# Optimization experiments

Measured on AMD Instinct MI355X. Metric: run time of the kernel, lower is better.

## Reference

```python
import jax, jax.numpy as jnp
import numpy as np

H = 64          # nheads
NH = 8          # lru_dim // nheads (per-head state dim, must be even)
LRU_DIM = 512
HIDDEN = 512
BATCH = 8
T = 4096
MAX_PHASE = 6.28
R_MIN, R_MAX = 0.9, 0.999


def setup_inputs() -> dict:
    key = jax.random.key(0)
    ks = jax.random.split(key, 8)
    input_sequence = jax.random.normal(ks[0], (BATCH, 1, HIDDEN, 1, T), dtype=jnp.float32)
    # theta_init: log(uniform(0, max_phase)), shape (lru_dim//2, 1)
    theta_log = jnp.log(jax.random.uniform(ks[1], (LRU_DIM // 2, 1), maxval=MAX_PHASE))
    # ortho_mat_init(lru_dim, N)
    P = jax.random.normal(ks[2], (LRU_DIM, NH)) / jnp.sqrt(NH + LRU_DIM)
    # mat_init(lru_dim, hidden_dim)
    B = jax.random.normal(ks[3], (LRU_DIM, HIDDEN)) / jnp.sqrt(HIDDEN + LRU_DIM)
    # mat_init(hidden_dim, lru_dim)
    C = jax.random.normal(ks[4], (HIDDEN, LRU_DIM)) / jnp.sqrt(HIDDEN + LRU_DIM)
    D = jax.random.normal(ks[5], (HIDDEN,))
    # nu_log_init: log(-log r) interpolated by uniform
    u1 = jax.random.uniform(ks[6], (H,))
    gamma_log = jnp.log(-jnp.log(R_MAX)) + u1 * (jnp.log(-jnp.log(R_MIN)) - jnp.log(-jnp.log(R_MAX)))
    return dict(input_sequence=input_sequence, theta_log=theta_log, P=P, B=B, C=C, D=D,
                gamma_log=gamma_log)


def _mix_sequence(gamma, thetas, Us):
    """Single head. gamma: scalar, thetas: (N/2,), Us: (T, B, N) -> (T, B, N)."""
    def binf(a, b):
        g_i, th_i, acc_i = a
        g_j, th_j, acc_j = b
        # rotate-half (RoPE-style) of accumulated state
        rot = jnp.stack([-acc_i[..., 1::2], acc_i[..., 0::2]], axis=-1).reshape(acc_i.shape)
        theta = jnp.repeat(th_j[..., None], 2, axis=-1).reshape(th_j.shape[:-1] + (th_j.shape[-1] * 2,))
        sin = jnp.sin(theta)[..., None, :]  # (..., 1, N)
        cos = jnp.cos(theta)[..., None, :]
        acc = g_j[..., None, None] * (cos * acc_i + sin * rot)
        return (g_i * g_j, th_i + th_j, acc + acc_j)

    Tlen = Us.shape[0]
    gammas = jnp.repeat(gamma[None], Tlen, axis=0)          # (T,)
    Rs = jnp.repeat(thetas[None, :], Tlen, axis=0)          # (T, N/2)
    _, _, res = jax.lax.associative_scan(binf, (gammas, Rs, Us))
    return res


def reference(input_sequence, theta_log, P, B, C, D, gamma_log):
    x = input_sequence[:, 0, :, 0].transpose(0, 2, 1)       # (B, T, hidden)
    bsz, Tlen, _ = x.shape
    thetas = jnp.exp(theta_log.reshape(H, NH // 2))          # (H, N/2)
    Pm = P.reshape(H, NH, NH)
    Bm = B.reshape(H, NH, HIDDEN)
    gamma = jnp.exp(-jnp.exp(gamma_log))                     # (H,)
    # trace(B B^T) per head == sum of squares
    trace_per_head = jnp.sum(Bm * Bm, axis=(1, 2))
    norm = jnp.sqrt((1.0 - gamma ** 2) / trace_per_head)
    B_norm = norm[:, None, None] * Bm                        # (H, N, hidden)
    # orthogonalize P via matrix exponential of skew-symmetric part
    Pm = jax.vmap(jax.scipy.linalg.expm)(Pm - Pm.transpose(0, 2, 1))  # (H, N, N)
    Us = jnp.einsum('HnD,BTD->HTBn', B_norm, x)              # project inputs per head
    Us = jnp.einsum('HnN,HTBn->HTBN', Pm.transpose(0, 2, 1), Us)
    y = jax.vmap(_mix_sequence)(gamma, thetas, Us)           # (H, T, B, N)
    y = jnp.einsum('HNn,HTBN->HTBn', Pm, y)
    y = y.transpose(2, 1, 0, 3).reshape(bsz, Tlen, -1)       # (B, T, lru_dim)
    y = jnp.einsum('Dn,BTn->BTD', C, y) + D * x
    return y[0]                                              # (T, hidden)
```

## Files before the change

### kernel.cpp

```cpp
#include <hip/hip_runtime.h>
#include <math.h>

#define NHEADS   64
#define TLEN     4096
#define CHUNK    16
#define NCHUNK   256

typedef unsigned short u16;
typedef unsigned int   u32;
typedef __attribute__((ext_vector_type(8))) short bf16x8;
typedef __attribute__((ext_vector_type(4))) float f32x4;

__device__ __forceinline__ u16 f2bf(float x) {
    u32 u = __float_as_uint(x);
    u32 r = (u + 0x7FFFu + ((u >> 16) & 1u)) >> 16;
    return (u16)r;
}
__device__ __forceinline__ float bf2f(u16 h) { return __uint_as_float(((u32)h) << 16); }


__global__ void k_setup(const float* __restrict__ P,
                        const float* __restrict__ Bmat,
                        const float* __restrict__ theta_log,
                        const float* __restrict__ gamma_log,
                        float* __restrict__ ws) {
    __shared__ double As[8][8];
    __shared__ double Rs[8][8];
    __shared__ double red[64];
    __shared__ int sh_s;
    const int h = blockIdx.x;
    const int tid = threadIdx.x;
    const int i = tid >> 3, j = tid & 7;

    As[i][j] = (double)P[(h*8 + i)*8 + j] - (double)P[(h*8 + j)*8 + i];

    const float* Bh = Bmat + h*8*512;
    double ss = 0.0;
    for (int q = 0; q < 64; ++q) { float v = Bh[q*64 + tid]; ss += (double)v * (double)v; }
    red[tid] = ss;
    __syncthreads();

    if (tid == 0) {
        double nrm = 0.0;
        for (int r = 0; r < 8; ++r) {
            double rs = 0.0;
            for (int c = 0; c < 8; ++c) rs += fabs(As[r][c]);
            nrm = fmax(nrm, rs);
        }
        int s = 0;
        while (nrm > 0.25 && s < 40) { nrm *= 0.5; ++s; }
        sh_s = s;
        double tr = 0.0;
        for (int q = 0; q < 64; ++q) tr += red[q];
        double ed = exp((double)gamma_log[h]);
        double g  = exp(-ed);
        ws[4096 + h] = (float)g;
        ws[4416 + h] = (float)sqrt((1.0 - g*g) / tr);
    }
    if (tid < 4) ws[4160 + h*4 + tid] = expf(theta_log[h*4 + tid]);
    __syncthreads();

    const double sc = ldexp(1.0, -sh_s);
    As[i][j] *= sc;
    const int NT = 13;
    Rs[i][j] = (i == j ? 1.0 : 0.0) + As[i][j] / (double)NT;
    __syncthreads();
    for (int k = NT - 1; k >= 1; --k) {
        double t = 0.0;
        #pragma unroll
        for (int m = 0; m < 8; ++m) t += As[i][m] * Rs[m][j];
        __syncthreads();
        Rs[i][j] = (i == j ? 1.0 : 0.0) + t / (double)k;
        __syncthreads();
    }
    for (int q = 0; q < sh_s; ++q) {
        double t = 0.0;
        #pragma unroll
        for (int m = 0; m < 8; ++m) t += Rs[i][m] * Rs[m][j];
        __syncthreads();
        Rs[i][j] = t;
        __syncthreads();
    }
    ws[h*64 + i*8 + j] = (float)Rs[i][j];
}

__global__ void k_proj(const float* __restrict__ Bmat,
                       const float* __restrict__ C,
                       const float* __restrict__ ws_ro,
                       u16* __restrict__ W1pk,
                       u16* __restrict__ CEpk) {
    const int gid = blockIdx.x * 256 + threadIdx.x;
    if (gid < 512*512) {
        const int k = gid >> 9, d = gid & 511;
        const int h = k >> 3, N = k & 7;
        const float* Pm = ws_ro + h*64 + N*8;
        const float nrm = ws_ro[4416 + h];
        float acc = 0.f;
        #pragma unroll
        for (int n = 0; n < 8; ++n) acc += Pm[n] * Bmat[(h*8 + n)*512 + d];
        acc *= nrm;
        u16 hi = f2bf(acc), lo = f2bf(acc - bf2f(hi));
        W1pk[k*1024 + d] = hi;
        W1pk[k*1024 + 512 + d] = lo;
    } else {
        const int g2 = gid - 512*512;
        const int e = g2 >> 9, k = g2 & 511;
        const int h = k >> 3, N = k & 7;
        const float* Pm = ws_ro + h*64 + N*8;
        float acc = 0.f;
        #pragma unroll
        for (int n = 0; n < 8; ++n) acc += Pm[n] * C[e*512 + h*8 + n];
        u16 hi = f2bf(acc), lo = f2bf(acc - bf2f(hi));
        CEpk[e*1024 + k] = hi;
        CEpk[e*1024 + 512 + k] = lo;
    }
}

__global__ void k_xt(const float* __restrict__ X, u16* __restrict__ XT) {
    __shared__ float Xs[64][65];
    const int tid = threadIdx.x;
    const int t0 = blockIdx.x * 64, d0 = blockIdx.y * 64;
    {
        const int dr = tid >> 4, tc = (tid & 15) * 4;
        #pragma unroll
        for (int it = 0; it < 4; ++it) {
            const int dd = it*16 + dr;
            float4 v = *reinterpret_cast<const float4*>(X + (size_t)(d0 + dd)*4096 + t0 + tc);
            Xs[dd][tc] = v.x; Xs[dd][tc+1] = v.y; Xs[dd][tc+2] = v.z; Xs[dd][tc+3] = v.w;
        }
    }
    __syncthreads();
    const int tr = tid >> 2, ds = (tid & 3) * 16;
    u32 hb[8], lb[8];
    #pragma unroll
    for (int j = 0; j < 16; j += 2) {
        float a = Xs[ds + j][tr], b = Xs[ds + j + 1][tr];
        u16 ha = f2bf(a), la = f2bf(a - bf2f(ha));
        u16 hbb = f2bf(b), lbb = f2bf(b - bf2f(hbb));
        hb[j >> 1] = (u32)ha | ((u32)hbb << 16);
        lb[j >> 1] = (u32)la | ((u32)lbb << 16);
    }
    u16* orow = XT + (size_t)(t0 + tr)*1024 + d0 + ds;
    uint4 h0; h0.x = hb[0]; h0.y = hb[1]; h0.z = hb[2]; h0.w = hb[3];
    uint4 h1; h1.x = hb[4]; h1.y = hb[5]; h1.z = hb[6]; h1.w = hb[7];
    uint4 l0; l0.x = lb[0]; l0.y = lb[1]; l0.z = lb[2]; l0.w = lb[3];
    uint4 l1; l1.x = lb[4]; l1.y = lb[5]; l1.z = lb[6]; l1.w = lb[7];
    *reinterpret_cast<uint4*>(orow)       = h0;
    *reinterpret_cast<uint4*>(orow + 8)   = h1;
    *reinterpret_cast<uint4*>(orow + 512) = l0;
    *reinterpret_cast<uint4*>(orow + 520) = l1;
}

#define MFMA_BF16(A_, B_, C_) __builtin_amdgcn_mfma_f32_16x16x32_bf16(A_, B_, C_, 0, 0, 0)
template<int MODE>
__global__ __launch_bounds__(256) void k_gemm(const u16* __restrict__ Apk,
                                              const float* __restrict__ Af,
                                              const u16* __restrict__ Bpk,
                                              float* __restrict__ Cout,
                                              const u16* __restrict__ XT,
                                              const float* __restrict__ Dvec,
                                              const float* __restrict__ wsro,
                                              float* __restrict__ E,
                                              const float* __restrict__ S,
                                              const float* __restrict__ TAB) {
    __shared__ char smem[36864];
    u16* Ah = (u16*)smem;
    u16* Al = Ah + 4608;
    u16* Bh = Al + 4608;
    u16* Bl = Bh + 4608;
    float* Ut = (float*)smem;

    const int tid = threadIdx.x;
    const int bid = blockIdx.x;
    const int tile = (bid & 7) * 64 + (bid >> 3);
    const int mt = tile >> 3, nt = tile & 7;
    const int m0 = mt * 64, n0 = nt * 64;
    const int lane = tid & 63, wid = tid >> 6;
    const int wm = wid >> 1, wn = wid & 1;
    const int lr = lane & 15, lc = lane >> 4;
    const int sr = tid >> 2, ss = (tid & 3) * 16;

    f32x4 acc00 = {0.f,0.f,0.f,0.f}, acc01 = acc00, acc10 = acc00, acc11 = acc00;

    const int tA = m0 + sr;
    const int cA = tA >> 4, iA = tA & 15;
    const u16* Brow = Bpk + (size_t)(n0 + sr)*1024 + ss;
    const u16* Arow = (MODE == 0) ? (Apk + (size_t)tA*1024 + ss) : (const u16*)0;
    const float* Urow = (MODE == 1) ? (Af + (size_t)tA*512 + ss) : (const float*)0;

    for (int k0 = 0; k0 < 512; k0 += 64) {
        float4 vbh0 = *reinterpret_cast<const float4*>(Brow + k0);
        float4 vbh1 = *reinterpret_cast<const float4*>(Brow + k0 + 8);
        float4 vbl0 = *reinterpret_cast<const float4*>(Brow + 512 + k0);
        float4 vbl1 = *reinterpret_cast<const float4*>(Brow + 512 + k0 + 8);
        if constexpr (MODE == 0) {
            float4 vah0 = *reinterpret_cast<const float4*>(Arow + k0);
            float4 vah1 = *reinterpret_cast<const float4*>(Arow + k0 + 8);
            float4 val0 = *reinterpret_cast<const float4*>(Arow + 512 + k0);
            float4 val1 = *reinterpret_cast<const float4*>(Arow + 512 + k0 + 8);
            *reinterpret_cast<float4*>(&Ah[sr*72 + ss])     = vah0;
            *reinterpret_cast<float4*>(&Ah[sr*72 + ss + 8]) = vah1;
            *reinterpret_cast<float4*>(&Al[sr*72 + ss])     = val0;
            *reinterpret_cast<float4*>(&Al[sr*72 + ss + 8]) = val1;
        } else {
            const int p0 = (k0 + ss) >> 1;
            #pragma unroll
            for (int j = 0; j < 4; ++j) {
                float4 u = *reinterpret_cast<const float4*>(Urow + k0 + 4*j);
                float4 tb = *reinterpret_cast<const float4*>(TAB + ((size_t)iA*256 + p0 + 2*j)*2);
                float4 sv = *reinterpret_cast<const float4*>(S + (size_t)cA*512 + 2*p0 + 4*j);
                u.x += tb.x*sv.x - tb.y*sv.y;
                u.y += tb.y*sv.x + tb.x*sv.y;
                u.z += tb.z*sv.z - tb.w*sv.w;
                u.w += tb.w*sv.z + tb.z*sv.w;
                u16 hx = f2bf(u.x), hy = f2bf(u.y), hz = f2bf(u.z), hw = f2bf(u.w);
                u16 lx = f2bf(u.x - bf2f(hx)), ly = f2bf(u.y - bf2f(hy));
                u16 lz = f2bf(u.z - bf2f(hz)), lw = f2bf(u.w - bf2f(hw));
                uint2 wh; wh.x = (u32)hx | ((u32)hy << 16); wh.y = (u32)hz | ((u32)hw << 16);
                uint2 wl; wl.x = (u32)lx | ((u32)ly << 16); wl.y = (u32)lz | ((u32)lw << 16);
                *reinterpret_cast<uint2*>(&Ah[sr*72 + ss + 4*j]) = wh;
                *reinterpret_cast<uint2*>(&Al[sr*72 + ss + 4*j]) = wl;
            }
        }
        *reinterpret_cast<float4*>(&Bh[sr*72 + ss])     = vbh0;
        *reinterpret_cast<float4*>(&Bh[sr*72 + ss + 8]) = vbh1;
        *reinterpret_cast<float4*>(&Bl[sr*72 + ss])     = vbl0;
        *reinterpret_cast<float4*>(&Bl[sr*72 + ss + 8]) = vbl1;
        __syncthreads();
        #pragma unroll
        for (int kk = 0; kk < 2; ++kk) {
            const int ko = kk*32 + lc*8;
            const int ra0 = (wm*32 + lr)*72 + ko,  ra1 = ra0 + 16*72;
            const int rb0 = (wn*32 + lr)*72 + ko,  rb1 = rb0 + 16*72;
            bf16x8 fah0 = *reinterpret_cast<const bf16x8*>(&Ah[ra0]);
            bf16x8 fah1 = *reinterpret_cast<const bf16x8*>(&Ah[ra1]);
            bf16x8 fal0 = *reinterpret_cast<const bf16x8*>(&Al[ra0]);
            bf16x8 fal1 = *reinterpret_cast<const bf16x8*>(&Al[ra1]);
            bf16x8 fbh0 = *reinterpret_cast<const bf16x8*>(&Bh[rb0]);
            bf16x8 fbh1 = *reinterpret_cast<const bf16x8*>(&Bh[rb1]);
            bf16x8 fbl0 = *reinterpret_cast<const bf16x8*>(&Bl[rb0]);
            bf16x8 fbl1 = *reinterpret_cast<const bf16x8*>(&Bl[rb1]);
            acc00 = MFMA_BF16(fah0, fbl0, acc00);
            acc00 = MFMA_BF16(fal0, fbh0, acc00);
            acc00 = MFMA_BF16(fah0, fbh0, acc00);
            acc01 = MFMA_BF16(fah0, fbl1, acc01);
            acc01 = MFMA_BF16(fal0, fbh1, acc01);
            acc01 = MFMA_BF16(fah0, fbh1, acc01);
            acc10 = MFMA_BF16(fah1, fbl0, acc10);
            acc10 = MFMA_BF16(fal1, fbh0, acc10);
            acc10 = MFMA_BF16(fah1, fbh0, acc10);
            acc11 = MFMA_BF16(fah1, fbl1, acc11);
            acc11 = MFMA_BF16(fal1, fbh1, acc11);
            acc11 = MFMA_BF16(fah1, fbh1, acc11);
        }
        __syncthreads();
    }

    if constexpr (MODE == 0) {
        #pragma unroll
        for (int im = 0; im < 2; ++im) {
            #pragma unroll
            for (int in = 0; in < 2; ++in) {
                f32x4 v = (im == 0) ? (in == 0 ? acc00 : acc01)
                                    : (in == 0 ? acc10 : acc11);
                const int row0 = wm*32 + im*16 + lc*4;
                const int col  = wn*32 + in*16 + lr;
                #pragma unroll
                for (int rg = 0; rg < 4; ++rg)
                    Ut[(row0 + rg)*72 + col] = v[rg];
            }
        }
        __syncthreads();
        if (tid < 128) {
            const int cc = tid >> 5, pp = tid & 31;
            const int pg = nt*32 + pp;
            const float th = wsro[4160 + pg];
            const float g  = wsro[4096 + (pg >> 2)];
            const float cs = cosf(th), sn = sinf(th);
            float h0 = 0.f, h1 = 0.f;
            float* col = Ut + (cc*16)*72 + 2*pp;
            #pragma unroll
            for (int i = 0; i < CHUNK; ++i) {
                float a = col[i*72], b = col[i*72 + 1];
                float n0v = g*(cs*h0 - sn*h1) + a;
                float n1v = g*(sn*h0 + cs*h1) + b;
                col[i*72] = n0v; col[i*72 + 1] = n1v;
                h0 = n0v; h1 = n1v;
            }
            E[(size_t)(mt*4 + cc)*512 + 2*pg]     = h0;
            E[(size_t)(mt*4 + cc)*512 + 2*pg + 1] = h1;
        }
        __syncthreads();
        const int row = tid >> 2, cseg = (tid & 3) * 16;
        #pragma unroll
        for (int j = 0; j < 4; ++j) {
            float4 v = *reinterpret_cast<const float4*>(&Ut[row*72 + cseg + 4*j]);
            *reinterpret_cast<float4*>(Cout + (size_t)(m0 + row)*512 + n0 + cseg + 4*j) = v;
        }
    } else {
        #pragma unroll
        for (int im = 0; im < 2; ++im) {
            #pragma unroll
            for (int in = 0; in < 2; ++in) {
                f32x4 v = (im == 0) ? (in == 0 ? acc00 : acc01)
                                    : (in == 0 ? acc10 : acc11);
                const int row0 = m0 + wm*32 + im*16 + lc*4;
                const int col  = n0 + wn*32 + in*16 + lr;
                const float dv = Dvec[col];
                #pragma unroll
                for (int rg = 0; rg < 4; ++rg) {
                    const int t = row0 + rg;
                    float xv = bf2f(XT[(size_t)t*1024 + col]) + bf2f(XT[(size_t)t*1024 + 512 + col]);
                    Cout[(size_t)t*512 + col] = v[rg] + dv*xv;
                }
            }
        }
    }
}

__global__ void k_carry(const float* __restrict__ E, float* __restrict__ S,
                        float* __restrict__ TAB,
                        const float* __restrict__ theta_log,
                        const float* __restrict__ gamma_log) {
    const int p = threadIdx.x;
    const double th = exp((double)theta_log[p]);
    const double ed = exp((double)gamma_log[p >> 2]);
    const double g  = exp(-ed);
    const double cd = cos(th), sd = sin(th);
    double gc = g*cd, gs = g*sd;
    for (int i = 0; i < CHUNK; ++i) {
        if (i) {
            double t0 = g*(cd*gc - sd*gs);
            double t1 = g*(sd*gc + cd*gs);
            gc = t0; gs = t1;
        }
        TAB[(i*256 + p)*2 + 0] = (float)gc;
        TAB[(i*256 + p)*2 + 1] = (float)gs;
    }
    const float fLc = (float)gc, fLs = (float)gs;
    float s0 = 0.f, s1 = 0.f;
    S[2*p] = 0.f; S[2*p + 1] = 0.f;
    const float* Ep = E + 2*p;
    float* Sp = S + 2*p;
    float2 bA[16], bB[16];
    #pragma unroll
    for (int j = 0; j < 16; ++j) bA[j] = *reinterpret_cast<const float2*>(Ep + (size_t)j*512);
    for (int bb = 0; bb < 8; ++bb) {
        const int b0 = 2*bb, b1 = 2*bb + 1;
        #pragma unroll
        for (int j = 0; j < 16; ++j)
            bB[j] = *reinterpret_cast<const float2*>(Ep + (size_t)(b1*16 + j)*512);
        #pragma unroll
        for (int j = 0; j < 16; ++j) {
            const int c = b0*16 + j + 1;
            float n0 = fLc*s0 - fLs*s1 + bA[j].x;
            float n1 = fLs*s0 + fLc*s1 + bA[j].y;
            s0 = n0; s1 = n1;
            *reinterpret_cast<float2*>(Sp + (size_t)c*512) = make_float2(s0, s1);
        }
        if (b1 + 1 < 16) {
            #pragma unroll
            for (int j = 0; j < 16; ++j)
                bA[j] = *reinterpret_cast<const float2*>(Ep + (size_t)((b1 + 1)*16 + j)*512);
        }
        #pragma unroll
        for (int j = 0; j < 16; ++j) {
            const int c = b1*16 + j + 1;
            float n0 = fLc*s0 - fLs*s1 + bB[j].x;
            float n1 = fLs*s0 + fLc*s1 + bB[j].y;
            s0 = n0; s1 = n1;
            if (c < NCHUNK)
                *reinterpret_cast<float2*>(Sp + (size_t)c*512) = make_float2(s0, s1);
        }
    }
}

extern "C" void kernel_launch(void* const* d_in, const int* in_sizes, int n_in,
                              void* d_out, int out_size, void* d_ws, size_t ws_size,
                              hipStream_t stream) {
    const float* X  = (const float*)d_in[0];
    const float* th = (const float*)d_in[1];
    const float* P  = (const float*)d_in[2];
    const float* Bm = (const float*)d_in[3];
    const float* C  = (const float*)d_in[4];
    const float* Dv = (const float*)d_in[5];
    const float* gl = (const float*)d_in[6];
    char* wsb = (char*)d_ws;
    float* ws   = (float*)wsb;
    u16*   W1pk = (u16*)(wsb + 32768);
    u16*   CEpk = (u16*)(wsb + 1081344);
    u16*   XTpk = (u16*)(wsb + 2129920);
    float* U    = (float*)(wsb + 10518528);
    float* E    = (float*)(wsb + 18907136);
    float* S    = (float*)(wsb + 19431424);
    float* TAB  = (float*)(wsb + 19955712);
    float* out  = (float*)d_out;

    k_setup<<<NHEADS, 64, 0, stream>>>(P, Bm, th, gl, ws);
    k_proj<<<2048, 256, 0, stream>>>(Bm, C, ws, W1pk, CEpk);
    k_xt<<<dim3(64, 8), 256, 0, stream>>>(X, XTpk);
    k_gemm<0><<<512, 256, 0, stream>>>(XTpk, (const float*)0, W1pk, U, XTpk, Dv, ws, E, S, TAB);
    k_carry<<<1, 256, 0, stream>>>(E, S, TAB, th, gl);
    k_gemm<1><<<512, 256, 0, stream>>>((const u16*)0, U, CEpk, out, XTpk, Dv, ws, E, S, TAB);
}
```

Measured before the change: 161.0 us.

## Parallelize chunk carry scan, fuse setup with transpose, prefetch GEMM tiles

The single-block serial carry recurrence over 256 chunks becomes a 64-block kernel with one wavefront per state pair. It runs a wave-level Kogge-Stone scan using shuffles and computes decay powers in closed form. The setup and input-transpose kernels merge into one launch, and the GEMM main loop register-prefetches the next K tile while MFMA runs on the current one. These target the serial latency of the carry kernel, one launch overhead, and global-load stalls in the GEMM. The trade-offs are extra transcendental work and slightly different float rounding in the scan.

Result: faster. 149.1 us (-7.4%).

```diff
diff --git a/kernel.cpp b/kernel.cpp
--- a/kernel.cpp
+++ b/kernel.cpp
@@ -19,24 +19,62 @@
 __device__ __forceinline__ float bf2f(u16 h) { return __uint_as_float(((u32)h) << 16); }
 
 
-__global__ void k_setup(const float* __restrict__ P,
-                        const float* __restrict__ Bmat,
-                        const float* __restrict__ theta_log,
-                        const float* __restrict__ gamma_log,
-                        float* __restrict__ ws) {
+__global__ void k_pre(const float* __restrict__ X, u16* __restrict__ XT,
+                      const float* __restrict__ P,
+                      const float* __restrict__ Bmat,
+                      const float* __restrict__ theta_log,
+                      const float* __restrict__ gamma_log,
+                      float* __restrict__ ws) {
+    const int tid = threadIdx.x;
+    if (blockIdx.x < 512) {
+        __shared__ float Xs[64][65];
+        const int t0 = (blockIdx.x & 63) * 64, d0 = (blockIdx.x >> 6) * 64;
+        {
+            const int dr = tid >> 4, tc = (tid & 15) * 4;
+            #pragma unroll
+            for (int it = 0; it < 4; ++it) {
+                const int dd = it*16 + dr;
+                float4 v = *reinterpret_cast<const float4*>(X + (size_t)(d0 + dd)*4096 + t0 + tc);
+                Xs[dd][tc] = v.x; Xs[dd][tc+1] = v.y; Xs[dd][tc+2] = v.z; Xs[dd][tc+3] = v.w;
+            }
+        }
+        __syncthreads();
+        const int tr = tid >> 2, ds = (tid & 3) * 16;
+        u32 hb[8], lb[8];
+        #pragma unroll
+        for (int j = 0; j < 16; j += 2) {
+            float a = Xs[ds + j][tr], b = Xs[ds + j + 1][tr];
+            u16 ha = f2bf(a), la = f2bf(a - bf2f(ha));
+            u16 hbb = f2bf(b), lbb = f2bf(b - bf2f(hbb));
+            hb[j >> 1] = (u32)ha | ((u32)hbb << 16);
+            lb[j >> 1] = (u32)la | ((u32)lbb << 16);
+        }
+        u16* orow = XT + (size_t)(t0 + tr)*1024 + d0 + ds;
+        uint4 h0; h0.x = hb[0]; h0.y = hb[1]; h0.z = hb[2]; h0.w = hb[3];
+        uint4 h1; h1.x = hb[4]; h1.y = hb[5]; h1.z = hb[6]; h1.w = hb[7];
+        uint4 l0; l0.x = lb[0]; l0.y = lb[1]; l0.z = lb[2]; l0.w = lb[3];
+        uint4 l1; l1.x = lb[4]; l1.y = lb[5]; l1.z = lb[6]; l1.w = lb[7];
+        *reinterpret_cast<uint4*>(orow)       = h0;
+        *reinterpret_cast<uint4*>(orow + 8)   = h1;
+        *reinterpret_cast<uint4*>(orow + 512) = l0;
+        *reinterpret_cast<uint4*>(orow + 520) = l1;
+        return;
+    }
     __shared__ double As[8][8];
     __shared__ double Rs[8][8];
-    __shared__ double red[64];
+    __shared__ double red[256];
     __shared__ int sh_s;
-    const int h = blockIdx.x;
-    const int tid = threadIdx.x;
-    const int i = tid >> 3, j = tid & 7;
-
-    As[i][j] = (double)P[(h*8 + i)*8 + j] - (double)P[(h*8 + j)*8 + i];
+    const int h = blockIdx.x - 512;
+    const int i = (tid & 63) >> 3, j = tid & 7;
+    const bool act = tid < 64;
+
+    if (act)
+        As[i][j] = (double)P[(h*8 + i)*8 + j] - (double)P[(h*8 + j)*8 + i];
 
     const float* Bh = Bmat + h*8*512;
     double ss = 0.0;
-    for (int q = 0; q < 64; ++q) { float v = Bh[q*64 + tid]; ss += (double)v * (double)v; }
+    #pragma unroll
+    for (int q = 0; q < 16; ++q) { float v = Bh[q*256 + tid]; ss += (double)v * (double)v; }
     red[tid] = ss;
     __syncthreads();
 
@@ -51,7 +89,7 @@
         while (nrm > 0.25 && s < 40) { nrm *= 0.5; ++s; }
         sh_s = s;
         double tr = 0.0;
-        for (int q = 0; q < 64; ++q) tr += red[q];
+        for (int q = 0; q < 256; ++q) tr += red[q];
         double ed = exp((double)gamma_log[h]);
         double g  = exp(-ed);
         ws[4096 + h] = (float)g;
@@ -60,28 +98,35 @@
     if (tid < 4) ws[4160 + h*4 + tid] = expf(theta_log[h*4 + tid]);
     __syncthreads();
 
-    const double sc = ldexp(1.0, -sh_s);
-    As[i][j] *= sc;
     const int NT = 13;
-    Rs[i][j] = (i == j ? 1.0 : 0.0) + As[i][j] / (double)NT;
+    if (act) {
+        const double sc = ldexp(1.0, -sh_s);
+        As[i][j] *= sc;
+        Rs[i][j] = (i == j ? 1.0 : 0.0) + As[i][j] / (double)NT;
+    }
     __syncthreads();
     for (int k = NT - 1; k >= 1; --k) {
         double t = 0.0;
-        #pragma unroll
-        for (int m = 0; m < 8; ++m) t += As[i][m] * Rs[m][j];
-        __syncthreads();
-        Rs[i][j] = (i == j ? 1.0 : 0.0) + t / (double)k;
-        __syncthreads();
-    }
-    for (int q = 0; q < sh_s; ++q) {
+        if (act) {
+            #pragma unroll
+            for (int m = 0; m < 8; ++m) t += As[i][m] * Rs[m][j];
+        }
+        __syncthreads();
+        if (act) Rs[i][j] = (i == j ? 1.0 : 0.0) + t / (double)k;
+        __syncthreads();
+    }
+    const int nsq = sh_s;
+    for (int q = 0; q < nsq; ++q) {
         double t = 0.0;
-        #pragma unroll
-        for (int m = 0; m < 8; ++m) t += Rs[i][m] * Rs[m][j];
-        __syncthreads();
-        Rs[i][j] = t;
-        __syncthreads();
-    }
-    ws[h*64 + i*8 + j] = (float)Rs[i][j];
+        if (act) {
+            #pragma unroll
+            for (int m = 0; m < 8; ++m) t += Rs[i][m] * Rs[m][j];
+        }
+        __syncthreads();
+        if (act) Rs[i][j] = t;
+        __syncthreads();
+    }
+    if (act) ws[h*64 + i*8 + j] = (float)Rs[i][j];
 }
 
 __global__ void k_proj(const float* __restrict__ Bmat,
@@ -114,41 +159,6 @@
         CEpk[e*1024 + k] = hi;
         CEpk[e*1024 + 512 + k] = lo;
     }
-}
-
-__global__ void k_xt(const float* __restrict__ X, u16* __restrict__ XT) {
-    __shared__ float Xs[64][65];
-    const int tid = threadIdx.x;
-    const int t0 = blockIdx.x * 64, d0 = blockIdx.y * 64;
-    {
-        const int dr = tid >> 4, tc = (tid & 15) * 4;
-        #pragma unroll
-        for (int it = 0; it < 4; ++it) {
-            const int dd = it*16 + dr;
-            float4 v = *reinterpret_cast<const float4*>(X + (size_t)(d0 + dd)*4096 + t0 + tc);
-            Xs[dd][tc] = v.x; Xs[dd][tc+1] = v.y; Xs[dd][tc+2] = v.z; Xs[dd][tc+3] = v.w;
-        }
-    }
-    __syncthreads();
-    const int tr = tid >> 2, ds = (tid & 3) * 16;
-    u32 hb[8], lb[8];
-    #pragma unroll
-    for (int j = 0; j < 16; j += 2) {
-        float a = Xs[ds + j][tr], b = Xs[ds + j + 1][tr];
-        u16 ha = f2bf(a), la = f2bf(a - bf2f(ha));
-        u16 hbb = f2bf(b), lbb = f2bf(b - bf2f(hbb));
-        hb[j >> 1] = (u32)ha | ((u32)hbb << 16);
-        lb[j >> 1] = (u32)la | ((u32)lbb << 16);
-    }
-    u16* orow = XT + (size_t)(t0 + tr)*1024 + d0 + ds;
-    uint4 h0; h0.x = hb[0]; h0.y = hb[1]; h0.z = hb[2]; h0.w = hb[3];
-    uint4 h1; h1.x = hb[4]; h1.y = hb[5]; h1.z = hb[6]; h1.w = hb[7];
-    uint4 l0; l0.x = lb[0]; l0.y = lb[1]; l0.z = lb[2]; l0.w = lb[3];
-    uint4 l1; l1.x = lb[4]; l1.y = lb[5]; l1.z = lb[6]; l1.w = lb[7];
-    *reinterpret_cast<uint4*>(orow)       = h0;
-    *reinterpret_cast<uint4*>(orow + 8)   = h1;
-    *reinterpret_cast<uint4*>(orow + 512) = l0;
-    *reinterpret_cast<uint4*>(orow + 520) = l1;
 }
 
 #define MFMA_BF16(A_, B_, C_) __builtin_amdgcn_mfma_f32_16x16x32_bf16(A_, B_, C_, 0, 0, 0)
@@ -188,27 +198,42 @@
     const u16* Arow = (MODE == 0) ? (Apk + (size_t)tA*1024 + ss) : (const u16*)0;
     const float* Urow = (MODE == 1) ? (Af + (size_t)tA*512 + ss) : (const float*)0;
 
-    for (int k0 = 0; k0 < 512; k0 += 64) {
-        float4 vbh0 = *reinterpret_cast<const float4*>(Brow + k0);
-        float4 vbh1 = *reinterpret_cast<const float4*>(Brow + k0 + 8);
-        float4 vbl0 = *reinterpret_cast<const float4*>(Brow + 512 + k0);
-        float4 vbl1 = *reinterpret_cast<const float4*>(Brow + 512 + k0 + 8);
+    float4 rb0, rb1, rb2, rb3;
+    float4 ra0, ra1, ra2, ra3;
+    float4 ru[4], rtb[4], rsv[4];
+
+    {
+        const int k0 = 0;
+        rb0 = *reinterpret_cast<const float4*>(Brow + k0);
+        rb1 = *reinterpret_cast<const float4*>(Brow + k0 + 8);
+        rb2 = *reinterpret_cast<const float4*>(Brow + 512 + k0);
+        rb3 = *reinterpret_cast<const float4*>(Brow + 512 + k0 + 8);
         if constexpr (MODE == 0) {
-            float4 vah0 = *reinterpret_cast<const float4*>(Arow + k0);
-            float4 vah1 = *reinterpret_cast<const float4*>(Arow + k0 + 8);
-            float4 val0 = *reinterpret_cast<const float4*>(Arow + 512 + k0);
-            float4 val1 = *reinterpret_cast<const float4*>(Arow + 512 + k0 + 8);
-            *reinterpret_cast<float4*>(&Ah[sr*72 + ss])     = vah0;
-            *reinterpret_cast<float4*>(&Ah[sr*72 + ss + 8]) = vah1;
-            *reinterpret_cast<float4*>(&Al[sr*72 + ss])     = val0;
-            *reinterpret_cast<float4*>(&Al[sr*72 + ss + 8]) = val1;
+            ra0 = *reinterpret_cast<const float4*>(Arow + k0);
+            ra1 = *reinterpret_cast<const float4*>(Arow + k0 + 8);
+            ra2 = *reinterpret_cast<const float4*>(Arow + 512 + k0);
+            ra3 = *reinterpret_cast<const float4*>(Arow + 512 + k0 + 8);
         } else {
             const int p0 = (k0 + ss) >> 1;
             #pragma unroll
             for (int j = 0; j < 4; ++j) {
-                float4 u = *reinterpret_cast<const float4*>(Urow + k0 + 4*j);
-                float4 tb = *reinterpret_cast<const float4*>(TAB + ((size_t)iA*256 + p0 + 2*j)*2);
-                float4 sv = *reinterpret_cast<const float4*>(S + (size_t)cA*512 + 2*p0 + 4*j);
+                ru[j]  = *reinterpret_cast<const float4*>(Urow + k0 + 4*j);
+                rtb[j] = *reinterpret_cast<const float4*>(TAB + ((size_t)iA*256 + p0 + 2*j)*2);
+                rsv[j] = *reinterpret_cast<const float4*>(S + (size_t)cA*512 + 2*p0 + 4*j);
+            }
+        }
+    }
+
+    for (int s = 0; s < 8; ++s) {
+        if constexpr (MODE == 0) {
+            *reinterpret_cast<float4*>(&Ah[sr*72 + ss])     = ra0;
+            *reinterpret_cast<float4*>(&Ah[sr*72 + ss + 8]) = ra1;
+            *reinterpret_cast<float4*>(&Al[sr*72 + ss])     = ra2;
+            *reinterpret_cast<float4*>(&Al[sr*72 + ss + 8]) = ra3;
+        } else {
+            #pragma unroll
+            for (int j = 0; j < 4; ++j) {
+                float4 u = ru[j], tb = rtb[j], sv = rsv[j];
                 u.x += tb.x*sv.x - tb.y*sv.y;
                 u.y += tb.y*sv.x + tb.x*sv.y;
                 u.z += tb.z*sv.z - tb.w*sv.w;
@@ -222,24 +247,47 @@
                 *reinterpret_cast<uint2*>(&Al[sr*72 + ss + 4*j]) = wl;
             }
         }
-        *reinterpret_cast<float4*>(&Bh[sr*72 + ss])     = vbh0;
-        *reinterpret_cast<float4*>(&Bh[sr*72 + ss + 8]) = vbh1;
-        *reinterpret_cast<float4*>(&Bl[sr*72 + ss])     = vbl0;
-        *reinterpret_cast<float4*>(&Bl[sr*72 + ss + 8]) = vbl1;
-        __syncthreads();
+        *reinterpret_cast<float4*>(&Bh[sr*72 + ss])     = rb0;
+        *reinterpret_cast<float4*>(&Bh[sr*72 + ss + 8]) = rb1;
+        *reinterpret_cast<float4*>(&Bl[sr*72 + ss])     = rb2;
+        *reinterpret_cast<float4*>(&Bl[sr*72 + ss + 8]) = rb3;
+        __syncthreads();
+
+        if (s < 7) {
+            const int k0 = (s + 1) * 64;
+            rb0 = *reinterpret_cast<const float4*>(Brow + k0);
+            rb1 = *reinterpret_cast<const float4*>(Brow + k0 + 8);
+            rb2 = *reinterpret_cast<const float4*>(Brow + 512 + k0);
+            rb3 = *reinterpret_cast<const float4*>(Brow + 512 + k0 + 8);
+            if constexpr (MODE == 0) {
+                ra0 = *reinterpret_cast<const float4*>(Arow + k0);
+                ra1 = *reinterpret_cast<const float4*>(Arow + k0 + 8);
+                ra2 = *reinterpret_cast<const float4*>(Arow + 512 + k0);
+                ra3 = *reinterpret_cast<const float4*>(Arow + 512 + k0 + 8);
+            } else {
+                const int p0 = (k0 + ss) >> 1;
+                #pragma unroll
+                for (int j = 0; j < 4; ++j) {
+                    ru[j]  = *reinterpret_cast<const float4*>(Urow + k0 + 4*j);
+                    rtb[j] = *reinterpret_cast<const float4*>(TAB + ((size_t)iA*256 + p0 + 2*j)*2);
+                    rsv[j] = *reinterpret_cast<const float4*>(S + (size_t)cA*512 + 2*p0 + 4*j);
+                }
+            }
+        }
+
         #pragma unroll
         for (int kk = 0; kk < 2; ++kk) {
             const int ko = kk*32 + lc*8;
-            const int ra0 = (wm*32 + lr)*72 + ko,  ra1 = ra0 + 16*72;
-            const int rb0 = (wn*32 + lr)*72 + ko,  rb1 = rb0 + 16*72;
-            bf16x8 fah0 = *reinterpret_cast<const bf16x8*>(&Ah[ra0]);
-            bf16x8 fah1 = *reinterpret_cast<const bf16x8*>(&Ah[ra1]);
-            bf16x8 fal0 = *reinterpret_cast<const bf16x8*>(&Al[ra0]);
-            bf16x8 fal1 = *reinterpret_cast<const bf16x8*>(&Al[ra1]);
-            bf16x8 fbh0 = *reinterpret_cast<const bf16x8*>(&Bh[rb0]);
-            bf16x8 fbh1 = *reinterpret_cast<const bf16x8*>(&Bh[rb1]);
-            bf16x8 fbl0 = *reinterpret_cast<const bf16x8*>(&Bl[rb0]);
-            bf16x8 fbl1 = *reinterpret_cast<const bf16x8*>(&Bl[rb1]);
+            const int ra0i = (wm*32 + lr)*72 + ko,  ra1i = ra0i + 16*72;
+            const int rb0i = (wn*32 + lr)*72 + ko,  rb1i = rb0i + 16*72;
+            bf16x8 fah0 = *reinterpret_cast<const bf16x8*>(&Ah[ra0i]);
+            bf16x8 fah1 = *reinterpret_cast<const bf16x8*>(&Ah[ra1i]);
+            bf16x8 fal0 = *reinterpret_cast<const bf16x8*>(&Al[ra0i]);
+            bf16x8 fal1 = *reinterpret_cast<const bf16x8*>(&Al[ra1i]);
+            bf16x8 fbh0 = *reinterpret_cast<const bf16x8*>(&Bh[rb0i]);
+            bf16x8 fbh1 = *reinterpret_cast<const bf16x8*>(&Bh[rb1i]);
+            bf16x8 fbl0 = *reinterpret_cast<const bf16x8*>(&Bl[rb0i]);
+            bf16x8 fbl1 = *reinterpret_cast<const bf16x8*>(&Bl[rb1i]);
             acc00 = MFMA_BF16(fah0, fbl0, acc00);
             acc00 = MFMA_BF16(fal0, fbh0, acc00);
             acc00 = MFMA_BF16(fah0, fbh0, acc00);
@@ -322,57 +370,56 @@
                         float* __restrict__ TAB,
                         const float* __restrict__ theta_log,
                         const float* __restrict__ gamma_log) {
-    const int p = threadIdx.x;
+    const int w = threadIdx.x >> 6, l = threadIdx.x & 63;
+    const int p = blockIdx.x*4 + w;
     const double th = exp((double)theta_log[p]);
     const double ed = exp((double)gamma_log[p >> 2]);
-    const double g  = exp(-ed);
-    const double cd = cos(th), sd = sin(th);
-    double gc = g*cd, gs = g*sd;
-    for (int i = 0; i < CHUNK; ++i) {
-        if (i) {
-            double t0 = g*(cd*gc - sd*gs);
-            double t1 = g*(sd*gc + cd*gs);
-            gc = t0; gs = t1;
-        }
-        TAB[(i*256 + p)*2 + 0] = (float)gc;
-        TAB[(i*256 + p)*2 + 1] = (float)gs;
-    }
-    const float fLc = (float)gc, fLs = (float)gs;
-    float s0 = 0.f, s1 = 0.f;
-    S[2*p] = 0.f; S[2*p + 1] = 0.f;
+
+    if (l < CHUNK) {
+        double a = (double)(l + 1) * th;
+        double g = exp(-(double)(l + 1) * ed);
+        TAB[((size_t)l*256 + p)*2 + 0] = (float)(g * cos(a));
+        TAB[((size_t)l*256 + p)*2 + 1] = (float)(g * sin(a));
+    }
+
+    const double a16 = 16.0*th, g16 = exp(-16.0*ed);
+    const float Lc = (float)(g16*cos(a16)), Ls = (float)(g16*sin(a16));
+
     const float* Ep = E + 2*p;
+    float2 e0 = *reinterpret_cast<const float2*>(Ep + (size_t)(4*l + 0)*512);
+    float2 e1 = *reinterpret_cast<const float2*>(Ep + (size_t)(4*l + 1)*512);
+    float2 e2 = *reinterpret_cast<const float2*>(Ep + (size_t)(4*l + 2)*512);
+    float2 e3 = *reinterpret_cast<const float2*>(Ep + (size_t)(4*l + 3)*512);
+
+    float2 v = e0;
+    v = make_float2(Lc*v.x - Ls*v.y + e1.x, Ls*v.x + Lc*v.y + e1.y);
+    v = make_float2(Lc*v.x - Ls*v.y + e2.x, Ls*v.x + Lc*v.y + e2.y);
+    v = make_float2(Lc*v.x - Ls*v.y + e3.x, Ls*v.x + Lc*v.y + e3.y);
+
+    #pragma unroll
+    for (int d = 0; d < 6; ++d) {
+        const int sh = 1 << d;
+        const double aa = 64.0 * (double)sh * th;
+        const double gg = exp(-64.0 * (double)sh * ed);
+        const float Mc = (float)(gg*cos(aa)), Ms = (float)(gg*sin(aa));
+        float px = __shfl_up(v.x, sh, 64);
+        float py = __shfl_up(v.y, sh, 64);
+        if (l >= sh) {
+            v.x += Mc*px - Ms*py;
+            v.y += Ms*px + Mc*py;
+        }
+    }
+
+    float sx = __shfl_up(v.x, 1, 64), sy = __shfl_up(v.y, 1, 64);
+    float2 s = (l == 0) ? make_float2(0.f, 0.f) : make_float2(sx, sy);
     float* Sp = S + 2*p;
-    float2 bA[16], bB[16];
-    #pragma unroll
-    for (int j = 0; j < 16; ++j) bA[j] = *reinterpret_cast<const float2*>(Ep + (size_t)j*512);
-    for (int bb = 0; bb < 8; ++bb) {
-        const int b0 = 2*bb, b1 = 2*bb + 1;
-        #pragma unroll
-        for (int j = 0; j < 16; ++j)
-            bB[j] = *reinterpret_cast<const float2*>(Ep + (size_t)(b1*16 + j)*512);
-        #pragma unroll
-        for (int j = 0; j < 16; ++j) {
-            const int c = b0*16 + j + 1;
-            float n0 = fLc*s0 - fLs*s1 + bA[j].x;
-            float n1 = fLs*s0 + fLc*s1 + bA[j].y;
-            s0 = n0; s1 = n1;
-            *reinterpret_cast<float2*>(Sp + (size_t)c*512) = make_float2(s0, s1);
-        }
-        if (b1 + 1 < 16) {
-            #pragma unroll
-            for (int j = 0; j < 16; ++j)
-                bA[j] = *reinterpret_cast<const float2*>(Ep + (size_t)((b1 + 1)*16 + j)*512);
-        }
-        #pragma unroll
-        for (int j = 0; j < 16; ++j) {
-            const int c = b1*16 + j + 1;
-            float n0 = fLc*s0 - fLs*s1 + bB[j].x;
-            float n1 = fLs*s0 + fLc*s1 + bB[j].y;
-            s0 = n0; s1 = n1;
-            if (c < NCHUNK)
-                *reinterpret_cast<float2*>(Sp + (size_t)c*512) = make_float2(s0, s1);
-        }
-    }
+    *reinterpret_cast<float2*>(Sp + (size_t)(4*l + 0)*512) = s;
+    s = make_float2(Lc*s.x - Ls*s.y + e0.x, Ls*s.x + Lc*s.y + e0.y);
+    *reinterpret_cast<float2*>(Sp + (size_t)(4*l + 1)*512) = s;
+    s = make_float2(Lc*s.x - Ls*s.y + e1.x, Ls*s.x + Lc*s.y + e1.y);
+    *reinterpret_cast<float2*>(Sp + (size_t)(4*l + 2)*512) = s;
+    s = make_float2(Lc*s.x - Ls*s.y + e2.x, Ls*s.x + Lc*s.y + e2.y);
+    *reinterpret_cast<float2*>(Sp + (size_t)(4*l + 3)*512) = s;
 }
 
 extern "C" void kernel_launch(void* const* d_in, const int* in_sizes, int n_in,
@@ -396,10 +443,9 @@
     float* TAB  = (float*)(wsb + 19955712);
     float* out  = (float*)d_out;
 
-    k_setup<<<NHEADS, 64, 0, stream>>>(P, Bm, th, gl, ws);
+    k_pre<<<576, 256, 0, stream>>>(X, XTpk, P, Bm, th, gl, ws);
     k_proj<<<2048, 256, 0, stream>>>(Bm, C, ws, W1pk, CEpk);
-    k_xt<<<dim3(64, 8), 256, 0, stream>>>(X, XTpk);
     k_gemm<0><<<512, 256, 0, stream>>>(XTpk, (const float*)0, W1pk, U, XTpk, Dv, ws, E, S, TAB);
-    k_carry<<<1, 256, 0, stream>>>(E, S, TAB, th, gl);
+    k_carry<<<64, 256, 0, stream>>>(E, S, TAB, th, gl);
     k_gemm<1><<<512, 256, 0, stream>>>((const u16*)0, U, CEpk, out, XTpk, Dv, ws, E, S, TAB);
 }
```
